# Kernel tuning notes

Measured on AMD Instinct MI355X. Metric: run time of the kernel, lower is better.

## Reference

```python
import jax, jax.numpy as jnp
import numpy as np

T, B, D = 512, 32, 1024

def setup_inputs() -> dict:
    key = jax.random.key(0)
    ks = jax.random.split(key, 4)
    scale = 1.0 / np.sqrt(D)
    x = jax.random.normal(ks[0], (T, B, D), dtype=jnp.float32)
    h0 = jnp.zeros((B, D), dtype=jnp.float32)
    W_alpha = jax.random.normal(ks[1], (D, D), dtype=jnp.float32) * scale
    b_alpha = jnp.zeros((D,), dtype=jnp.float32)
    # W_h in torch is orthogonal * 0.3; approximate with scaled gaussian of matching norm
    W_h = jax.random.normal(ks[2], (D, D), dtype=jnp.float32) * (0.3 * scale)
    W_x = jax.random.normal(ks[3], (D, D), dtype=jnp.float32) * scale
    b = jnp.zeros((D,), dtype=jnp.float32)
    return {"x": x, "h0": h0, "W_alpha": W_alpha, "b_alpha": b_alpha,
            "W_h": W_h, "W_x": W_x, "b": b}

def reference(x, h0, W_alpha, b_alpha, W_h, W_x, b):
    # Precompute input-dependent projections for all timesteps (batched GEMM)
    alpha_x_all = jnp.einsum('tbd,ed->tbe', x, W_alpha) + b_alpha  # [T,B,D]
    Wx_all = jnp.einsum('tbd,ed->tbe', x, W_x)                     # [T,B,D]

    def step(h_prev, inp):
        alpha_x_t, wx_t = inp
        alpha = jax.nn.sigmoid(alpha_x_t)
        v = jnp.tanh(h_prev @ W_h.T + wx_t + b)
        h_new = h_prev + alpha * v  # residual: identity path always present
        return h_new, h_new

    _, h_seq = jax.lax.scan(step, h0, (alpha_x_all, Wx_all))  # [T,B,D]
    h = jnp.concatenate([h0[None], h_seq], axis=0)            # [T+1,B,D]
    output = h_seq * jax.nn.silu(h_seq)                       # h * silu(h)
    return output, h
```

## Files before the change

kernel.cpp:

```cpp
#include <hip/hip_runtime.h>

typedef __bf16 bf16x8 __attribute__((ext_vector_type(8)));
typedef float  f32x4  __attribute__((ext_vector_type(4)));
typedef unsigned short u16;
typedef unsigned int   u32;
typedef unsigned long long u64;
typedef u16 u16x8 __attribute__((ext_vector_type(8)));

#define TT 512
#define BB 32
#define DD 1024

#define WS_Z   0
#define WS_HX  134217728
#define WS_FLG (134217728+262144)

static __device__ __forceinline__ u16 f2b(float f){
  u32 u = __builtin_bit_cast(u32, f);
  u32 r = (u + 0x7fffu + ((u>>16)&1u)) >> 16;
  return (u16)r;
}
static __device__ __forceinline__ float b2f(u16 h){
  return __builtin_bit_cast(float, (u32)h<<16);
}

#define AL32(p)   __hip_atomic_load((p),      __ATOMIC_RELAXED, __HIP_MEMORY_SCOPE_AGENT)
#define AL64(p)   __hip_atomic_load((p),      __ATOMIC_RELAXED, __HIP_MEMORY_SCOPE_AGENT)
#define AS32(p,v) __hip_atomic_store((p),(v), __ATOMIC_RELAXED, __HIP_MEMORY_SCOPE_AGENT)

#define MFMA16(a,b,c) __builtin_amdgcn_mfma_f32_16x16x32_bf16(a,b,c,0,0,0)

__global__ __launch_bounds__(256) void k_gemm3(const float* __restrict__ X,
    const float* __restrict__ Wa, const float* __restrict__ Wx,
    float* __restrict__ Z){
  __shared__ u16 Ahi[128*64];
  __shared__ u16 Alo[128*64];
  __shared__ u16 Bhi[128*64];
  __shared__ u16 Blo[128*64];
  int id  = blockIdx.x;
  int swz = (id & 7)*256 + (id>>3);
  int mblk = swz>>4, nblk = swz&15;
  const float* W = (nblk < 8) ? Wa : Wx;
  int n0 = (nblk&7)*128;
  int m0 = mblk*128;
  int tid = threadIdx.x, lane = tid&63, w = tid>>6;
  int wm = w>>1, wn = w&1;
  int sr = tid>>1, sh = tid&1;

  f32x4 acc[4][4];
  #pragma unroll
  for (int i=0;i<4;i++)
    #pragma unroll
    for (int j=0;j<4;j++) acc[i][j] = (f32x4){0.f,0.f,0.f,0.f};

  for (int kb = 0; kb < DD; kb += 64){
    const float* sa  = X + (size_t)(m0+sr)*DD + kb + sh*32;
    const float* sbp = W + (size_t)(n0+sr)*DD + kb + sh*32;
    int rswz = (sr&7)<<4;
    #pragma unroll
    for (int g=0; g<4; g++){
      float4 va0 = ((const float4*)sa)[g*2];
      float4 va1 = ((const float4*)sa)[g*2+1];
      float4 vb0 = ((const float4*)sbp)[g*2];
      float4 vb1 = ((const float4*)sbp)[g*2+1];
      float fa[8] = {va0.x,va0.y,va0.z,va0.w,va1.x,va1.y,va1.z,va1.w};
      float fb[8] = {vb0.x,vb0.y,vb0.z,vb0.w,vb1.x,vb1.y,vb1.z,vb1.w};
      u16x8 ah, al, bh, bl;
      #pragma unroll
      for (int j=0;j<8;j++){
        u16 ha = f2b(fa[j]); ah[j] = ha; al[j] = f2b(fa[j] - b2f(ha));
        u16 hb = f2b(fb[j]); bh[j] = hb; bl[j] = f2b(fb[j] - b2f(hb));
      }
      int off = sr*128 + ((sh*64 + g*16) ^ rswz);
      *(u16x8*)((char*)Ahi + off) = ah;
      *(u16x8*)((char*)Alo + off) = al;
      *(u16x8*)((char*)Bhi + off) = bh;
      *(u16x8*)((char*)Blo + off) = bl;
    }
    __syncthreads();
    #pragma unroll
    for (int ks=0; ks<2; ks++){
      int kby = ks*64 + ((lane>>4)<<4);
      bf16x8 ahf[4], alf[4], bhf[4], blf[4];
      #pragma unroll
      for (int mi=0;mi<4;mi++){
        int row = wm*64 + mi*16 + (lane&15);
        int ao = row*128 + (kby ^ ((row&7)<<4));
        ahf[mi] = *(const bf16x8*)((const char*)Ahi + ao);
        alf[mi] = *(const bf16x8*)((const char*)Alo + ao);
      }
      #pragma unroll
      for (int ni=0;ni<4;ni++){
        int row = wn*64 + ni*16 + (lane&15);
        int bo = row*128 + (kby ^ ((row&7)<<4));
        bhf[ni] = *(const bf16x8*)((const char*)Bhi + bo);
        blf[ni] = *(const bf16x8*)((const char*)Blo + bo);
      }
      #pragma unroll
      for (int mi=0;mi<4;mi++)
        #pragma unroll
        for (int ni=0;ni<4;ni++){
          acc[mi][ni] = MFMA16(ahf[mi], bhf[ni], acc[mi][ni]);
          acc[mi][ni] = MFMA16(ahf[mi], blf[ni], acc[mi][ni]);
          acc[mi][ni] = MFMA16(alf[mi], bhf[ni], acc[mi][ni]);
        }
    }
    __syncthreads();
  }

  #pragma unroll
  for (int mi=0;mi<4;mi++){
    #pragma unroll
    for (int ni=0;ni<4;ni++){
      int colz = nblk*128 + wn*64 + ni*16 + (lane&15);
      #pragma unroll
      for (int q=0;q<4;q++){
        int rowm = m0 + wm*64 + mi*16 + ((lane>>4)<<2) + q;
        Z[(size_t)rowm*2048 + colz] = acc[mi][ni][q];
      }
    }
  }
}

__global__ void k_init(const float* __restrict__ h0, float* __restrict__ hout0,
                       u32* __restrict__ hx, u32* __restrict__ flg){
  int i = blockIdx.x*blockDim.x + threadIdx.x;
  if (i < BB*DD){
    float v = h0[i];
    hout0[i] = v;
    u16 hh = f2b(v);
    u16 ll = f2b(v - b2f(hh));
    hx[i] = (u32)hh | ((u32)ll<<16);
  }
  if (i < 32) flg[i] = 0u;
  if (i == 32) flg[1024] = 0u;
}

#define UNPK(c, A, B) do { \
  u16x8 hi8, lo8; \
  hi8[0]=(u16)A.x; lo8[0]=(u16)(A.x>>16); \
  hi8[1]=(u16)A.y; lo8[1]=(u16)(A.y>>16); \
  hi8[2]=(u16)A.z; lo8[2]=(u16)(A.z>>16); \
  hi8[3]=(u16)A.w; lo8[3]=(u16)(A.w>>16); \
  hi8[4]=(u16)B.x; lo8[4]=(u16)(B.x>>16); \
  hi8[5]=(u16)B.y; lo8[5]=(u16)(B.y>>16); \
  hi8[6]=(u16)B.z; lo8[6]=(u16)(B.z>>16); \
  hi8[7]=(u16)B.w; lo8[7]=(u16)(B.w>>16); \
  int off_ = srow*2048 + ((kseg*128 + (c)*16) ^ ssw); \
  *(u16x8*)((char*)Hhi + off_) = hi8; \
  *(u16x8*)((char*)Hlo + off_) = lo8; \
} while(0)

__global__ __launch_bounds__(512, 2) void k_recur9(
    const float* __restrict__ Z, const float* __restrict__ Wh,
    const float* __restrict__ h0,
    const float* __restrict__ balpha, const float* __restrict__ bvec,
    float* __restrict__ out0,
    float* __restrict__ hout,
    u32* __restrict__ hx,
    u32* __restrict__ flg){
  __shared__ u16 Hhi[BB*DD];
  __shared__ u16 Hlo[BB*DD];
  __shared__ f32x4 Red[4][64];
  __shared__ int sdone;

  int blk = blockIdx.x;
  int tid = threadIdx.x, lane = tid&63, w = tid>>6;

  if (blk >= 32){
    if (tid == 0) sdone = 0;
    __syncthreads();
    float a = (float)tid + 1.0f;
    float m = 1.000001f, c = 0.9999991f;
    for (;;){
      for (int i = 0; i < 512; i++){
        asm volatile("v_fmac_f32 %0, %1, %2" : "+v"(a) : "v"(m), "v"(c));
      }
      if (tid == 0) sdone = (int)AL32(flg + 1024);
      __syncthreads();
      if (sdone) break;
      __syncthreads();
    }
    asm volatile("" :: "v"(a));
    return;
  }

  int e0 = blk*32;
  int kh = w>>2, wm = (w>>1)&1, wn = w&1;

  bf16x8 wfh[16], wfl[16];
  {
    const float* wrow = Wh + (size_t)(e0 + wn*16 + (lane&15))*DD
                           + kh*512 + ((lane>>4)<<3);
    #pragma unroll
    for (int ks=0; ks<16; ks++){
      float4 a = ((const float4*)(wrow + ks*32))[0];
      float4 b = ((const float4*)(wrow + ks*32))[1];
      float f[8] = {a.x,a.y,a.z,a.w,b.x,b.y,b.z,b.w};
      u16x8 uh, ul;
      #pragma unroll
      for (int j=0;j<8;j++){
        u16 hh = f2b(f[j]);
        uh[j] = hh;
        ul[j] = f2b(f[j] - b2f(hh));
      }
      wfh[ks] = __builtin_bit_cast(bf16x8, uh);
      wfl[ks] = __builtin_bit_cast(bf16x8, ul);
    }
  }

  int el = e0 + wn*16 + (lane&15);
  float ba = balpha[el], bb = bvec[el];
  float hc[4]  = {0.f,0.f,0.f,0.f};
  float ov[4]  = {0.f,0.f,0.f,0.f};
  float axr[4] = {0.f,0.f,0.f,0.f};
  float wxr[4] = {0.f,0.f,0.f,0.f};
  if (kh == 0){
    #pragma unroll
    for (int q=0;q<4;q++){
      int b = wm*16 + ((lane>>4)<<2) + q;
      hc[q]  = h0[b*DD + el];
      axr[q] = Z[(size_t)b*2048 + el];
      wxr[q] = Z[(size_t)b*2048 + DD + el];
    }
  }

  int srow = tid & 31;
  int kseg = tid >> 5;
  int ssw  = (srow & 15) << 4;

  for (int t=0;t<TT;t++){
    if (tid < 16){
      const u64* fp = (const u64*)(flg + tid*2);
      u64 fl = AL64(fp);
      while ((u32)fl < (u32)t || (u32)(fl>>32) < (u32)t) fl = AL64(fp);
    }
    __syncthreads();

    const u32* hsrc = hx + (size_t)(t&1)*BB*DD;
    const void* gp = (const void*)(hsrc + srow*DD + kseg*64);
    uint4 r0,r1,r2,r3,r4,r5,r6,r7,r8,r9,rA,rB,rC,rD,rE,rF;
    asm volatile(
      "global_load_dwordx4 %0, %16, off sc1\n\t"
      "global_load_dwordx4 %1, %16, off offset:16 sc1\n\t"
      "global_load_dwordx4 %2, %16, off offset:32 sc1\n\t"
      "global_load_dwordx4 %3, %16, off offset:48 sc1\n\t"
      "global_load_dwordx4 %4, %16, off offset:64 sc1\n\t"
      "global_load_dwordx4 %5, %16, off offset:80 sc1\n\t"
      "global_load_dwordx4 %6, %16, off offset:96 sc1\n\t"
      "global_load_dwordx4 %7, %16, off offset:112 sc1\n\t"
      "global_load_dwordx4 %8, %16, off offset:128 sc1\n\t"
      "global_load_dwordx4 %9, %16, off offset:144 sc1\n\t"
      "global_load_dwordx4 %10, %16, off offset:160 sc1\n\t"
      "global_load_dwordx4 %11, %16, off offset:176 sc1\n\t"
      "global_load_dwordx4 %12, %16, off offset:192 sc1\n\t"
      "global_load_dwordx4 %13, %16, off offset:208 sc1\n\t"
      "global_load_dwordx4 %14, %16, off offset:224 sc1\n\t"
      "global_load_dwordx4 %15, %16, off offset:240 sc1\n\t"
      "s_waitcnt vmcnt(0)"
      : "=&v"(r0), "=&v"(r1), "=&v"(r2), "=&v"(r3),
        "=&v"(r4), "=&v"(r5), "=&v"(r6), "=&v"(r7),
        "=&v"(r8), "=&v"(r9), "=&v"(rA), "=&v"(rB),
        "=&v"(rC), "=&v"(rD), "=&v"(rE), "=&v"(rF)
      : "v"(gp)
      : "memory");
    UNPK(0, r0, r1);  UNPK(1, r2, r3);
    UNPK(2, r4, r5);  UNPK(3, r6, r7);
    UNPK(4, r8, r9);  UNPK(5, rA, rB);
    UNPK(6, rC, rD);  UNPK(7, rE, rF);

    float axc[4], wxc[4];
    if (kh == 0){
      #pragma unroll
      for (int q=0;q<4;q++){ axc[q]=axr[q]; wxc[q]=wxr[q]; }
      if (t < TT-1){
        #pragma unroll
        for (int q=0;q<4;q++){
          int b = wm*16 + ((lane>>4)<<2) + q;
          size_t zi = ((size_t)(t+1)*BB + b)*2048 + el;
          axr[q] = Z[zi]; wxr[q] = Z[zi + DD];
        }
      }
    } else {
      #pragma unroll
      for (int q=0;q<4;q++){ axc[q]=0.f; wxc[q]=0.f; }
    }
    __syncthreads();

    f32x4 a0 = (f32x4){0.f,0.f,0.f,0.f};
    f32x4 a1 = (f32x4){0.f,0.f,0.f,0.f};
    f32x4 a2 = (f32x4){0.f,0.f,0.f,0.f};
    int ra    = wm*16 + (lane&15);
    int rbase = ra*2048;
    int rsw   = (ra&15)<<4;
    int kb0   = kh*1024 + ((lane>>4)<<4);
    #pragma unroll
    for (int ks=0; ks<16; ks++){
      int off = rbase + ((kb0 + ks*64) ^ rsw);
      bf16x8 ahi = *(const bf16x8*)((const char*)Hhi + off);
      bf16x8 alo = *(const bf16x8*)((const char*)Hlo + off);
      a0 = MFMA16(ahi, wfh[ks], a0);
      a1 = MFMA16(ahi, wfl[ks], a1);
      a2 = MFMA16(alo, wfh[ks], a2);
    }
    f32x4 acc = a0 + a1 + a2;
    if (kh == 1){ Red[wm*2+wn][lane] = acc; }
    __syncthreads();

    if (kh == 0){
      acc += Red[wm*2+wn][lane];
      u32* hnx = hx + (size_t)((t+1)&1)*BB*DD;
      #pragma unroll
      for (int q=0;q<4;q++){
        int b = wm*16 + ((lane>>4)<<2) + q;
        float ax = axc[q] + ba;
        float alpha = 1.f/(1.f + __expf(-ax));
        float s  = acc[q] + wxc[q] + bb;
        float as = fabsf(s);
        float e2 = __expf(-2.f*as);
        float vv = __builtin_copysignf((1.f - e2)/(1.f + e2), s);
        float h = hc[q] + alpha*vv;
        hc[q] = h;
        float sg = 1.f/(1.f + __expf(-h));
        ov[q] = h*h*sg;
        u16 hh = f2b(h);
        u16 ll = f2b(h - b2f(hh));
        AS32(hnx + b*DD + el, (u32)hh | ((u32)ll<<16));
      }
    }

    __syncthreads();
    if (tid == 0) AS32(flg + blk, (u32)(t+1));

    if (kh == 0){
      #pragma unroll
      for (int q=0;q<4;q++){
        int b = wm*16 + ((lane>>4)<<2) + q;
        size_t oi = (size_t)t*(BB*DD) + (size_t)b*DD + el;
        out0[oi] = ov[q];
        hout[oi + BB*DD] = hc[q];
      }
    }
  }

  if (tid == 0) AS32(flg + 1024, 1u);
}

extern "C" void kernel_launch(void* const* d_in, const int* in_sizes, int n_in,
                              void* d_out, int out_size, void* d_ws, size_t ws_size,
                              hipStream_t stream){
  (void)in_sizes; (void)n_in; (void)out_size; (void)ws_size;
  const float* x   = (const float*)d_in[0];
  const float* h0  = (const float*)d_in[1];
  const float* Wa  = (const float*)d_in[2];
  const float* bal = (const float*)d_in[3];
  const float* Whf = (const float*)d_in[4];
  const float* Wxf = (const float*)d_in[5];
  const float* bv  = (const float*)d_in[6];

  char* ws = (char*)d_ws;
  float* Zb  = (float*)(ws + WS_Z);
  u32*   hx  = (u32*)(ws + WS_HX);
  u32*   flg = (u32*)(ws + WS_FLG);

  float* out0 = (float*)d_out;
  float* hout = (float*)d_out + (size_t)TT*BB*DD;

  k_gemm3<<<2048, 256, 0, stream>>>(x, Wa, Wxf, Zb);
  k_init<<<(BB*DD+255)/256, 256, 0, stream>>>(h0, hout, hx, flg);

  void* args[] = {(void*)&Zb, (void*)&Whf, (void*)&h0, (void*)&bal, (void*)&bv,
                  (void*)&out0, (void*)&hout, (void*)&hx, (void*)&flg};
  hipLaunchCooperativeKernel((const void*)k_recur9, dim3(256), dim3(512),
                             args, 0, stream);
}
```

Measured before the change: 4.600 ms.

## Use single atomic counter barrier and overlap output stores with h loads

Replaces the per-block flag array, which 16 threads polled, with one global counter. Each wave that writes h increments it with an atomic add, and a single thread spins until the count reaches 128*t. The output and h stores for step t-1 are now issued after the next step's h loads, using a partial vmcnt wait so they overlap load latency, and the final step is stored after the loop. This also drops one __syncthreads per step, but adds contention on one atomic address and a dummy scratch buffer for t=0.

```diff
diff --git a/kernel.cpp b/kernel.cpp
--- a/kernel.cpp
+++ b/kernel.cpp
@@ -10,10 +10,12 @@
 #define TT 512
 #define BB 32
 #define DD 1024
+#define BBDD (BB*DD)
 
 #define WS_Z   0
 #define WS_HX  134217728
 #define WS_FLG (134217728+262144)
+#define WS_DMY (134217728+262144+8192)
 
 static __device__ __forceinline__ u16 f2b(float f){
   u32 u = __builtin_bit_cast(u32, f);
@@ -25,7 +27,6 @@
 }
 
 #define AL32(p)   __hip_atomic_load((p),      __ATOMIC_RELAXED, __HIP_MEMORY_SCOPE_AGENT)
-#define AL64(p)   __hip_atomic_load((p),      __ATOMIC_RELAXED, __HIP_MEMORY_SCOPE_AGENT)
 #define AS32(p,v) __hip_atomic_store((p),(v), __ATOMIC_RELAXED, __HIP_MEMORY_SCOPE_AGENT)
 
 #define MFMA16(a,b,c) __builtin_amdgcn_mfma_f32_16x16x32_bf16(a,b,c,0,0,0)
@@ -132,8 +133,8 @@
     u16 ll = f2b(v - b2f(hh));
     hx[i] = (u32)hh | ((u32)ll<<16);
   }
-  if (i < 32) flg[i] = 0u;
-  if (i == 32) flg[1024] = 0u;
+  if (i == 0) flg[0] = 0u;
+  if (i == 1) flg[1024] = 0u;
 }
 
 #define UNPK(c, A, B) do { \
@@ -151,14 +152,15 @@
   *(u16x8*)((char*)Hlo + off_) = lo8; \
 } while(0)
 
-__global__ __launch_bounds__(512, 2) void k_recur9(
+__global__ __launch_bounds__(512, 2) void k_recur11(
     const float* __restrict__ Z, const float* __restrict__ Wh,
     const float* __restrict__ h0,
     const float* __restrict__ balpha, const float* __restrict__ bvec,
     float* __restrict__ out0,
     float* __restrict__ hout,
     u32* __restrict__ hx,
-    u32* __restrict__ flg){
+    u32* __restrict__ flg,
+    float* __restrict__ dmy){
   __shared__ u16 Hhi[BB*DD];
   __shared__ u16 Hlo[BB*DD];
   __shared__ f32x4 Red[4][64];
@@ -230,10 +232,10 @@
   int ssw  = (srow & 15) << 4;
 
   for (int t=0;t<TT;t++){
-    if (tid < 16){
-      const u64* fp = (const u64*)(flg + tid*2);
-      u64 fl = AL64(fp);
-      while ((u32)fl < (u32)t || (u32)(fl>>32) < (u32)t) fl = AL64(fp);
+    if (tid == 256){
+      u32 tgt = 128u*(u32)t;
+      u32 c = AL32(flg);
+      while (c < tgt) c = AL32(flg);
     }
     __syncthreads();
 
@@ -256,14 +258,29 @@
       "global_load_dwordx4 %12, %16, off offset:192 sc1\n\t"
       "global_load_dwordx4 %13, %16, off offset:208 sc1\n\t"
       "global_load_dwordx4 %14, %16, off offset:224 sc1\n\t"
-      "global_load_dwordx4 %15, %16, off offset:240 sc1\n\t"
-      "s_waitcnt vmcnt(0)"
+      "global_load_dwordx4 %15, %16, off offset:240 sc1"
       : "=&v"(r0), "=&v"(r1), "=&v"(r2), "=&v"(r3),
         "=&v"(r4), "=&v"(r5), "=&v"(r6), "=&v"(r7),
         "=&v"(r8), "=&v"(r9), "=&v"(rA), "=&v"(rB),
         "=&v"(rC), "=&v"(rD), "=&v"(rE), "=&v"(rF)
       : "v"(gp)
       : "memory");
+
+    if (kh == 0){
+      float* o0 = (t == 0) ? dmy : (out0 + (size_t)(t-1)*BBDD);
+      float* h1 = (t == 0) ? (dmy + BBDD/2) : (hout + (size_t)t*BBDD);
+      #pragma unroll
+      for (int q=0;q<4;q++){
+        int b = wm*16 + ((lane>>4)<<2) + q;
+        o0[b*DD + el] = ov[q];
+        h1[b*DD + el] = hc[q];
+      }
+      asm volatile("s_waitcnt vmcnt(8)" ::: "memory");
+    } else {
+      asm volatile("s_waitcnt vmcnt(0)" ::: "memory");
+    }
+    __builtin_amdgcn_sched_barrier(0);
+
     UNPK(0, r0, r1);  UNPK(1, r2, r3);
     UNPK(2, r4, r5);  UNPK(3, r6, r7);
     UNPK(4, r8, r9);  UNPK(5, rA, rB);
@@ -273,13 +290,12 @@
     if (kh == 0){
       #pragma unroll
       for (int q=0;q<4;q++){ axc[q]=axr[q]; wxc[q]=wxr[q]; }
-      if (t < TT-1){
-        #pragma unroll
-        for (int q=0;q<4;q++){
-          int b = wm*16 + ((lane>>4)<<2) + q;
-          size_t zi = ((size_t)(t+1)*BB + b)*2048 + el;
-          axr[q] = Z[zi]; wxr[q] = Z[zi + DD];
-        }
+      int tn = (t < TT-1) ? (t+1) : t;
+      #pragma unroll
+      for (int q=0;q<4;q++){
+        int b = wm*16 + ((lane>>4)<<2) + q;
+        size_t zi = ((size_t)tn*BB + b)*2048 + el;
+        axr[q] = Z[zi]; wxr[q] = Z[zi + DD];
       }
     } else {
       #pragma unroll
@@ -327,22 +343,22 @@
         u16 ll = f2b(h - b2f(hh));
         AS32(hnx + b*DD + el, (u32)hh | ((u32)ll<<16));
       }
-    }
-
-    __syncthreads();
-    if (tid == 0) AS32(flg + blk, (u32)(t+1));
-
-    if (kh == 0){
-      #pragma unroll
-      for (int q=0;q<4;q++){
-        int b = wm*16 + ((lane>>4)<<2) + q;
-        size_t oi = (size_t)t*(BB*DD) + (size_t)b*DD + el;
-        out0[oi] = ov[q];
-        hout[oi + BB*DD] = hc[q];
-      }
-    }
-  }
-
+      asm volatile("s_waitcnt vmcnt(0)" ::: "memory");
+      if (lane == 0)
+        __hip_atomic_fetch_add(flg, 1u, __ATOMIC_RELAXED,
+                               __HIP_MEMORY_SCOPE_AGENT);
+    }
+  }
+
+  if (blk < 32 && (w>>2) == 0){
+    #pragma unroll
+    for (int q=0;q<4;q++){
+      int b = ((w>>1)&1)*16 + ((lane>>4)<<2) + q;
+      size_t oi = (size_t)(TT-1)*BBDD + (size_t)b*DD + el;
+      out0[oi] = ov[q];
+      hout[oi + BBDD] = hc[q];
+    }
+  }
   if (tid == 0) AS32(flg + 1024, 1u);
 }
 
@@ -362,6 +378,7 @@
   float* Zb  = (float*)(ws + WS_Z);
   u32*   hx  = (u32*)(ws + WS_HX);
   u32*   flg = (u32*)(ws + WS_FLG);
+  float* dmy = (float*)(ws + WS_DMY);
 
   float* out0 = (float*)d_out;
   float* hout = (float*)d_out + (size_t)TT*BB*DD;
@@ -370,7 +387,8 @@
   k_init<<<(BB*DD+255)/256, 256, 0, stream>>>(h0, hout, hx, flg);
 
   void* args[] = {(void*)&Zb, (void*)&Whf, (void*)&h0, (void*)&bal, (void*)&bv,
-                  (void*)&out0, (void*)&hout, (void*)&hx, (void*)&flg};
-  hipLaunchCooperativeKernel((const void*)k_recur9, dim3(256), dim3(512),
+                  (void*)&out0, (void*)&hout, (void*)&hx, (void*)&flg,
+                  (void*)&dmy};
+  hipLaunchCooperativeKernel((const void*)k_recur11, dim3(256), dim3(512),
                              args, 0, stream);
 }
```

After: 6.068 ms. 1.32x slower.

## Split recurrence block into independent batch-half groups with fine-grained flags

Applied to the files above, without the earlier changes.

Each 32-column block is split into two independent 4-wave groups, each handling 16 batch rows, with its own shared staging buffers. Block-wide __syncthreads are replaced by LDS counters and per-wave spin waits. Each group polls per-(group,block,wn) global flags with wave-wide __all and s_sleep, so the two batch halves can advance through time steps without waiting on each other. The reduction handoff between K-halves uses counter/ack pairs. This adds spin overhead and memory-ordering risk in exchange for less synchronisation latency on the critical path.

```diff
diff --git a/kernel.cpp b/kernel.cpp
--- a/kernel.cpp
+++ b/kernel.cpp
@@ -10,6 +10,7 @@
 #define TT 512
 #define BB 32
 #define DD 1024
+#define BBDD (BB*DD)
 
 #define WS_Z   0
 #define WS_HX  134217728
@@ -24,8 +25,8 @@
   return __builtin_bit_cast(float, (u32)h<<16);
 }
 
+#define AL64(p)   __hip_atomic_load((p),      __ATOMIC_RELAXED, __HIP_MEMORY_SCOPE_AGENT)
 #define AL32(p)   __hip_atomic_load((p),      __ATOMIC_RELAXED, __HIP_MEMORY_SCOPE_AGENT)
-#define AL64(p)   __hip_atomic_load((p),      __ATOMIC_RELAXED, __HIP_MEMORY_SCOPE_AGENT)
 #define AS32(p,v) __hip_atomic_store((p),(v), __ATOMIC_RELAXED, __HIP_MEMORY_SCOPE_AGENT)
 
 #define MFMA16(a,b,c) __builtin_amdgcn_mfma_f32_16x16x32_bf16(a,b,c,0,0,0)
@@ -58,11 +59,11 @@
     const float* sbp = W + (size_t)(n0+sr)*DD + kb + sh*32;
     int rswz = (sr&7)<<4;
     #pragma unroll
-    for (int g=0; g<4; g++){
-      float4 va0 = ((const float4*)sa)[g*2];
-      float4 va1 = ((const float4*)sa)[g*2+1];
-      float4 vb0 = ((const float4*)sbp)[g*2];
-      float4 vb1 = ((const float4*)sbp)[g*2+1];
+    for (int gg=0; gg<4; gg++){
+      float4 va0 = ((const float4*)sa)[gg*2];
+      float4 va1 = ((const float4*)sa)[gg*2+1];
+      float4 vb0 = ((const float4*)sbp)[gg*2];
+      float4 vb1 = ((const float4*)sbp)[gg*2+1];
       float fa[8] = {va0.x,va0.y,va0.z,va0.w,va1.x,va1.y,va1.z,va1.w};
       float fb[8] = {vb0.x,vb0.y,vb0.z,vb0.w,vb1.x,vb1.y,vb1.z,vb1.w};
       u16x8 ah, al, bh, bl;
@@ -71,7 +72,7 @@
         u16 ha = f2b(fa[j]); ah[j] = ha; al[j] = f2b(fa[j] - b2f(ha));
         u16 hb = f2b(fb[j]); bh[j] = hb; bl[j] = f2b(fb[j] - b2f(hb));
       }
-      int off = sr*128 + ((sh*64 + g*16) ^ rswz);
+      int off = sr*128 + ((sh*64 + gg*16) ^ rswz);
       *(u16x8*)((char*)Ahi + off) = ah;
       *(u16x8*)((char*)Alo + off) = al;
       *(u16x8*)((char*)Bhi + off) = bh;
@@ -132,8 +133,8 @@
     u16 ll = f2b(v - b2f(hh));
     hx[i] = (u32)hh | ((u32)ll<<16);
   }
-  if (i < 32) flg[i] = 0u;
-  if (i == 32) flg[1024] = 0u;
+  if (i < 128) flg[i] = 0u;
+  if (i == 128) flg[1024] = 0u;
 }
 
 #define UNPK(c, A, B) do { \
@@ -146,12 +147,12 @@
   hi8[5]=(u16)B.y; lo8[5]=(u16)(B.y>>16); \
   hi8[6]=(u16)B.z; lo8[6]=(u16)(B.z>>16); \
   hi8[7]=(u16)B.w; lo8[7]=(u16)(B.w>>16); \
-  int off_ = srow*2048 + ((kseg*128 + (c)*16) ^ ssw); \
-  *(u16x8*)((char*)Hhi + off_) = hi8; \
-  *(u16x8*)((char*)Hlo + off_) = lo8; \
+  int off_ = srow*2048 + ((kby0 + (c)*16) ^ ssw); \
+  *(u16x8*)(HhiB + off_) = hi8; \
+  *(u16x8*)(HloB + off_) = lo8; \
 } while(0)
 
-__global__ __launch_bounds__(512, 2) void k_recur9(
+__global__ __launch_bounds__(512, 2) void k_recur13(
     const float* __restrict__ Z, const float* __restrict__ Wh,
     const float* __restrict__ h0,
     const float* __restrict__ balpha, const float* __restrict__ bvec,
@@ -159,9 +160,12 @@
     float* __restrict__ hout,
     u32* __restrict__ hx,
     u32* __restrict__ flg){
-  __shared__ u16 Hhi[BB*DD];
-  __shared__ u16 Hlo[BB*DD];
-  __shared__ f32x4 Red[4][64];
+  __shared__ u16 Hhi[2][16*1024];
+  __shared__ u16 Hlo[2][16*1024];
+  __shared__ f32x4 Red[2][2][64];
+  __shared__ u32 StgCnt[2];
+  __shared__ u32 RedCnt[2][2];
+  __shared__ u32 RedAck[2][2];
   __shared__ int sdone;
 
   int blk = blockIdx.x;
@@ -185,8 +189,17 @@
     return;
   }
 
+  int g  = w>>2;
+  int kh = (w>>1)&1;
+  int wn = w&1;
   int e0 = blk*32;
-  int kh = w>>2, wm = (w>>1)&1, wn = w&1;
+
+  if (tid == 0){
+    StgCnt[0]=0; StgCnt[1]=0;
+    RedCnt[0][0]=0; RedCnt[0][1]=0; RedCnt[1][0]=0; RedCnt[1][1]=0;
+    RedAck[0][0]=0; RedAck[0][1]=0; RedAck[1][0]=0; RedAck[1][1]=0;
+  }
+  __syncthreads();
 
   bf16x8 wfh[16], wfl[16];
   {
@@ -212,33 +225,42 @@
   int el = e0 + wn*16 + (lane&15);
   float ba = balpha[el], bb = bvec[el];
   float hc[4]  = {0.f,0.f,0.f,0.f};
-  float ov[4]  = {0.f,0.f,0.f,0.f};
   float axr[4] = {0.f,0.f,0.f,0.f};
   float wxr[4] = {0.f,0.f,0.f,0.f};
   if (kh == 0){
     #pragma unroll
     for (int q=0;q<4;q++){
-      int b = wm*16 + ((lane>>4)<<2) + q;
+      int b = g*16 + ((lane>>4)<<2) + q;
       hc[q]  = h0[b*DD + el];
       axr[q] = Z[(size_t)b*2048 + el];
       wxr[q] = Z[(size_t)b*2048 + DD + el];
     }
   }
 
-  int srow = tid & 31;
-  int kseg = tid >> 5;
-  int ssw  = (srow & 15) << 4;
+  int srow  = lane&15;
+  int kbase = kh*512 + wn*256 + ((lane>>4)<<6);
+  int kby0  = kbase*2;
+  int ssw   = srow<<4;
+  char* HhiB = (char*)&Hhi[g][0];
+  char* HloB = (char*)&Hlo[g][0];
+  const u64* fp = (const u64*)(flg + g*64) + (lane&31);
+  volatile u32* stg = &StgCnt[g];
+  volatile u32* rcn = &RedCnt[g][wn];
+  volatile u32* rak = &RedAck[g][wn];
 
   for (int t=0;t<TT;t++){
-    if (tid < 16){
-      const u64* fp = (const u64*)(flg + tid*2);
-      u64 fl = AL64(fp);
-      while ((u32)fl < (u32)t || (u32)(fl>>32) < (u32)t) fl = AL64(fp);
-    }
-    __syncthreads();
-
-    const u32* hsrc = hx + (size_t)(t&1)*BB*DD;
-    const void* gp = (const void*)(hsrc + srow*DD + kseg*64);
+    {
+      u64 fv = AL64(fp);
+      int ok = ((u32)fv >= (u32)t) & ((u32)(fv>>32) >= (u32)t);
+      while (!__all(ok)){
+        __builtin_amdgcn_s_sleep(1);
+        fv = AL64(fp);
+        ok = ((u32)fv >= (u32)t) & ((u32)(fv>>32) >= (u32)t);
+      }
+    }
+
+    const u32* hsrc = hx + (size_t)(t&1)*BBDD;
+    const void* gp = (const void*)(hsrc + (g*16+srow)*DD + kbase);
     uint4 r0,r1,r2,r3,r4,r5,r6,r7,r8,r9,rA,rB,rC,rD,rE,rF;
     asm volatile(
       "global_load_dwordx4 %0, %16, off sc1\n\t"
@@ -264,58 +286,56 @@
         "=&v"(rC), "=&v"(rD), "=&v"(rE), "=&v"(rF)
       : "v"(gp)
       : "memory");
+    __builtin_amdgcn_sched_barrier(0);
     UNPK(0, r0, r1);  UNPK(1, r2, r3);
     UNPK(2, r4, r5);  UNPK(3, r6, r7);
     UNPK(4, r8, r9);  UNPK(5, rA, rB);
     UNPK(6, rC, rD);  UNPK(7, rE, rF);
 
-    float axc[4], wxc[4];
-    if (kh == 0){
-      #pragma unroll
-      for (int q=0;q<4;q++){ axc[q]=axr[q]; wxc[q]=wxr[q]; }
-      if (t < TT-1){
-        #pragma unroll
-        for (int q=0;q<4;q++){
-          int b = wm*16 + ((lane>>4)<<2) + q;
-          size_t zi = ((size_t)(t+1)*BB + b)*2048 + el;
-          axr[q] = Z[zi]; wxr[q] = Z[zi + DD];
-        }
-      }
-    } else {
-      #pragma unroll
-      for (int q=0;q<4;q++){ axc[q]=0.f; wxc[q]=0.f; }
-    }
-    __syncthreads();
+    asm volatile("s_waitcnt lgkmcnt(0)" ::: "memory");
+    if (lane == 0) atomicAdd((u32*)stg, 1u);
+    {
+      u32 tgt = 4u*(u32)(t+1);
+      while (*stg < tgt) __builtin_amdgcn_s_sleep(1);
+    }
+    __builtin_amdgcn_sched_barrier(0);
 
     f32x4 a0 = (f32x4){0.f,0.f,0.f,0.f};
     f32x4 a1 = (f32x4){0.f,0.f,0.f,0.f};
     f32x4 a2 = (f32x4){0.f,0.f,0.f,0.f};
-    int ra    = wm*16 + (lane&15);
-    int rbase = ra*2048;
-    int rsw   = (ra&15)<<4;
+    int rbase = (lane&15)*2048;
+    int rsw   = (lane&15)<<4;
     int kb0   = kh*1024 + ((lane>>4)<<4);
     #pragma unroll
     for (int ks=0; ks<16; ks++){
       int off = rbase + ((kb0 + ks*64) ^ rsw);
-      bf16x8 ahi = *(const bf16x8*)((const char*)Hhi + off);
-      bf16x8 alo = *(const bf16x8*)((const char*)Hlo + off);
+      bf16x8 ahi = *(const bf16x8*)(HhiB + off);
+      bf16x8 alo = *(const bf16x8*)(HloB + off);
       a0 = MFMA16(ahi, wfh[ks], a0);
       a1 = MFMA16(ahi, wfl[ks], a1);
       a2 = MFMA16(alo, wfh[ks], a2);
     }
     f32x4 acc = a0 + a1 + a2;
-    if (kh == 1){ Red[wm*2+wn][lane] = acc; }
-    __syncthreads();
-
-    if (kh == 0){
-      acc += Red[wm*2+wn][lane];
-      u32* hnx = hx + (size_t)((t+1)&1)*BB*DD;
+
+    if (kh == 1){
+      while (*rak < (u32)t) __builtin_amdgcn_s_sleep(1);
+      Red[g][wn][lane] = acc;
+      asm volatile("s_waitcnt lgkmcnt(0)" ::: "memory");
+      if (lane == 0) *rcn = (u32)(t+1);
+    } else {
+      while (*rcn < (u32)(t+1)) __builtin_amdgcn_s_sleep(1);
+      acc += Red[g][wn][lane];
+      asm volatile("s_waitcnt lgkmcnt(0)" ::: "memory");
+      if (lane == 0) *rak = (u32)(t+1);
+
+      float ov[4];
+      u32* hnx = hx + (size_t)((t+1)&1)*BBDD;
       #pragma unroll
       for (int q=0;q<4;q++){
-        int b = wm*16 + ((lane>>4)<<2) + q;
-        float ax = axc[q] + ba;
+        int b = g*16 + ((lane>>4)<<2) + q;
+        float ax = axr[q] + ba;
         float alpha = 1.f/(1.f + __expf(-ax));
-        float s  = acc[q] + wxc[q] + bb;
+        float s  = acc[q] + wxr[q] + bb;
         float as = fabsf(s);
         float e2 = __expf(-2.f*as);
         float vv = __builtin_copysignf((1.f - e2)/(1.f + e2), s);
@@ -327,23 +347,28 @@
         u16 ll = f2b(h - b2f(hh));
         AS32(hnx + b*DD + el, (u32)hh | ((u32)ll<<16));
       }
-    }
-
-    __syncthreads();
-    if (tid == 0) AS32(flg + blk, (u32)(t+1));
-
-    if (kh == 0){
+      asm volatile("s_waitcnt vmcnt(0)" ::: "memory");
+      if (lane == 0) AS32(flg + g*64 + blk*2 + wn, (u32)(t+1));
+
       #pragma unroll
       for (int q=0;q<4;q++){
-        int b = wm*16 + ((lane>>4)<<2) + q;
-        size_t oi = (size_t)t*(BB*DD) + (size_t)b*DD + el;
+        int b = g*16 + ((lane>>4)<<2) + q;
+        size_t oi = (size_t)t*BBDD + (size_t)b*DD + el;
         out0[oi] = ov[q];
-        hout[oi + BB*DD] = hc[q];
-      }
-    }
-  }
-
-  if (tid == 0) AS32(flg + 1024, 1u);
+        hout[oi + BBDD] = hc[q];
+      }
+      if (t < TT-1){
+        #pragma unroll
+        for (int q=0;q<4;q++){
+          int b = g*16 + ((lane>>4)<<2) + q;
+          size_t zi = ((size_t)(t+1)*BB + b)*2048 + el;
+          axr[q] = Z[zi]; wxr[q] = Z[zi + DD];
+        }
+      }
+    }
+  }
+
+  if (blk == 0 && tid == 0) AS32(flg + 1024, 1u);
 }
 
 extern "C" void kernel_launch(void* const* d_in, const int* in_sizes, int n_in,
@@ -371,6 +396,6 @@
 
   void* args[] = {(void*)&Zb, (void*)&Whf, (void*)&h0, (void*)&bal, (void*)&bv,
                   (void*)&out0, (void*)&hout, (void*)&hx, (void*)&flg};
-  hipLaunchCooperativeKernel((const void*)k_recur9, dim3(256), dim3(512),
+  hipLaunchCooperativeKernel((const void*)k_recur13, dim3(256), dim3(512),
                              args, 0, stream);
 }
```

New measurement: 7.106 ms. +54.5%, slower.

## Halve recurrence worker blocks to 16, each computing 64 columns over full batch

Applied to the files above, without the earlier changes.

The persistent recurrence now uses 16 worker blocks, each owning 64 output columns, instead of 32 blocks owning 32 columns. Each warp covers both batch halves with two MFMA fragment sets, and only 8 flag pairs are polled per step. The aim is to cut the cross-block synchronisation fan-in and the redundant per-block reloads of the full hidden state. The cost is twice the per-block MFMA and epilogue work on the serial critical path, plus more register pressure.

```diff
diff --git a/kernel.cpp b/kernel.cpp
--- a/kernel.cpp
+++ b/kernel.cpp
@@ -10,10 +10,12 @@
 #define TT 512
 #define BB 32
 #define DD 1024
+#define BBDD (BB*DD)
+#define NWB 16
 
 #define WS_Z   0
 #define WS_HX  134217728
-#define WS_FLG (134217728+262144)
+#define WS_FLG 134479872
 
 static __device__ __forceinline__ u16 f2b(float f){
   u32 u = __builtin_bit_cast(u32, f);
@@ -132,8 +134,8 @@
     u16 ll = f2b(v - b2f(hh));
     hx[i] = (u32)hh | ((u32)ll<<16);
   }
-  if (i < 32) flg[i] = 0u;
-  if (i == 32) flg[1024] = 0u;
+  if (i < NWB) flg[i] = 0u;
+  if (i == NWB) flg[1024] = 0u;
 }
 
 #define UNPK(c, A, B) do { \
@@ -151,7 +153,33 @@
   *(u16x8*)((char*)Hlo + off_) = lo8; \
 } while(0)
 
-__global__ __launch_bounds__(512, 2) void k_recur9(
+#define BURST16_SC1(GP) \
+    asm volatile( \
+      "global_load_dwordx4 %0, %16, off sc1\n\t" \
+      "global_load_dwordx4 %1, %16, off offset:16 sc1\n\t" \
+      "global_load_dwordx4 %2, %16, off offset:32 sc1\n\t" \
+      "global_load_dwordx4 %3, %16, off offset:48 sc1\n\t" \
+      "global_load_dwordx4 %4, %16, off offset:64 sc1\n\t" \
+      "global_load_dwordx4 %5, %16, off offset:80 sc1\n\t" \
+      "global_load_dwordx4 %6, %16, off offset:96 sc1\n\t" \
+      "global_load_dwordx4 %7, %16, off offset:112 sc1\n\t" \
+      "global_load_dwordx4 %8, %16, off offset:128 sc1\n\t" \
+      "global_load_dwordx4 %9, %16, off offset:144 sc1\n\t" \
+      "global_load_dwordx4 %10, %16, off offset:160 sc1\n\t" \
+      "global_load_dwordx4 %11, %16, off offset:176 sc1\n\t" \
+      "global_load_dwordx4 %12, %16, off offset:192 sc1\n\t" \
+      "global_load_dwordx4 %13, %16, off offset:208 sc1\n\t" \
+      "global_load_dwordx4 %14, %16, off offset:224 sc1\n\t" \
+      "global_load_dwordx4 %15, %16, off offset:240 sc1\n\t" \
+      "s_waitcnt vmcnt(0)" \
+      : "=&v"(r0), "=&v"(r1), "=&v"(r2), "=&v"(r3), \
+        "=&v"(r4), "=&v"(r5), "=&v"(r6), "=&v"(r7), \
+        "=&v"(r8), "=&v"(r9), "=&v"(rA), "=&v"(rB), \
+        "=&v"(rC), "=&v"(rD), "=&v"(rE), "=&v"(rF) \
+      : "v"(GP) \
+      : "memory")
+
+__global__ __launch_bounds__(512, 2) void k_recur15(
     const float* __restrict__ Z, const float* __restrict__ Wh,
     const float* __restrict__ h0,
     const float* __restrict__ balpha, const float* __restrict__ bvec,
@@ -161,13 +189,13 @@
     u32* __restrict__ flg){
   __shared__ u16 Hhi[BB*DD];
   __shared__ u16 Hlo[BB*DD];
-  __shared__ f32x4 Red[4][64];
+  __shared__ f32x4 Red[4][2][64];
   __shared__ int sdone;
 
   int blk = blockIdx.x;
   int tid = threadIdx.x, lane = tid&63, w = tid>>6;
 
-  if (blk >= 32){
+  if (blk >= NWB){
     if (tid == 0) sdone = 0;
     __syncthreads();
     float a = (float)tid + 1.0f;
@@ -185,8 +213,8 @@
     return;
   }
 
-  int e0 = blk*32;
-  int kh = w>>2, wm = (w>>1)&1, wn = w&1;
+  int e0 = blk*64;
+  int kh = w>>2, wn = w&3;
 
   bf16x8 wfh[16], wfl[16];
   {
@@ -211,18 +239,22 @@
 
   int el = e0 + wn*16 + (lane&15);
   float ba = balpha[el], bb = bvec[el];
-  float hc[4]  = {0.f,0.f,0.f,0.f};
-  float ov[4]  = {0.f,0.f,0.f,0.f};
-  float axr[4] = {0.f,0.f,0.f,0.f};
-  float wxr[4] = {0.f,0.f,0.f,0.f};
+  float hc[2][4], ov[2][4], axr[2][4], wxr[2][4];
+  #pragma unroll
+  for (int fr=0;fr<2;fr++)
+    #pragma unroll
+    for (int q=0;q<4;q++){ hc[fr][q]=0.f; ov[fr][q]=0.f;
+                           axr[fr][q]=0.f; wxr[fr][q]=0.f; }
   if (kh == 0){
     #pragma unroll
-    for (int q=0;q<4;q++){
-      int b = wm*16 + ((lane>>4)<<2) + q;
-      hc[q]  = h0[b*DD + el];
-      axr[q] = Z[(size_t)b*2048 + el];
-      wxr[q] = Z[(size_t)b*2048 + DD + el];
-    }
+    for (int fr=0;fr<2;fr++)
+      #pragma unroll
+      for (int q=0;q<4;q++){
+        int b = fr*16 + ((lane>>4)<<2) + q;
+        hc[fr][q]  = h0[b*DD + el];
+        axr[fr][q] = Z[(size_t)b*2048 + el];
+        wxr[fr][q] = Z[(size_t)b*2048 + DD + el];
+      }
   }
 
   int srow = tid & 31;
@@ -230,116 +262,111 @@
   int ssw  = (srow & 15) << 4;
 
   for (int t=0;t<TT;t++){
-    if (tid < 16){
+    if (tid < 8){
       const u64* fp = (const u64*)(flg + tid*2);
       u64 fl = AL64(fp);
       while ((u32)fl < (u32)t || (u32)(fl>>32) < (u32)t) fl = AL64(fp);
     }
     __syncthreads();
 
-    const u32* hsrc = hx + (size_t)(t&1)*BB*DD;
+    const u32* hsrc = hx + (size_t)(t&1)*BBDD;
     const void* gp = (const void*)(hsrc + srow*DD + kseg*64);
     uint4 r0,r1,r2,r3,r4,r5,r6,r7,r8,r9,rA,rB,rC,rD,rE,rF;
-    asm volatile(
-      "global_load_dwordx4 %0, %16, off sc1\n\t"
-      "global_load_dwordx4 %1, %16, off offset:16 sc1\n\t"
-      "global_load_dwordx4 %2, %16, off offset:32 sc1\n\t"
-      "global_load_dwordx4 %3, %16, off offset:48 sc1\n\t"
-      "global_load_dwordx4 %4, %16, off offset:64 sc1\n\t"
-      "global_load_dwordx4 %5, %16, off offset:80 sc1\n\t"
-      "global_load_dwordx4 %6, %16, off offset:96 sc1\n\t"
-      "global_load_dwordx4 %7, %16, off offset:112 sc1\n\t"
-      "global_load_dwordx4 %8, %16, off offset:128 sc1\n\t"
-      "global_load_dwordx4 %9, %16, off offset:144 sc1\n\t"
-      "global_load_dwordx4 %10, %16, off offset:160 sc1\n\t"
-      "global_load_dwordx4 %11, %16, off offset:176 sc1\n\t"
-      "global_load_dwordx4 %12, %16, off offset:192 sc1\n\t"
-      "global_load_dwordx4 %13, %16, off offset:208 sc1\n\t"
-      "global_load_dwordx4 %14, %16, off offset:224 sc1\n\t"
-      "global_load_dwordx4 %15, %16, off offset:240 sc1\n\t"
-      "s_waitcnt vmcnt(0)"
-      : "=&v"(r0), "=&v"(r1), "=&v"(r2), "=&v"(r3),
-        "=&v"(r4), "=&v"(r5), "=&v"(r6), "=&v"(r7),
-        "=&v"(r8), "=&v"(r9), "=&v"(rA), "=&v"(rB),
-        "=&v"(rC), "=&v"(rD), "=&v"(rE), "=&v"(rF)
-      : "v"(gp)
-      : "memory");
+    BURST16_SC1(gp);
     UNPK(0, r0, r1);  UNPK(1, r2, r3);
     UNPK(2, r4, r5);  UNPK(3, r6, r7);
     UNPK(4, r8, r9);  UNPK(5, rA, rB);
     UNPK(6, rC, rD);  UNPK(7, rE, rF);
 
-    float axc[4], wxc[4];
+    float axc[2][4], wxc[2][4];
     if (kh == 0){
       #pragma unroll
-      for (int q=0;q<4;q++){ axc[q]=axr[q]; wxc[q]=wxr[q]; }
+      for (int fr=0;fr<2;fr++)
+        #pragma unroll
+        for (int q=0;q<4;q++){ axc[fr][q]=axr[fr][q]; wxc[fr][q]=wxr[fr][q]; }
       if (t < TT-1){
         #pragma unroll
+        for (int fr=0;fr<2;fr++)
+          #pragma unroll
+          for (int q=0;q<4;q++){
+            int b = fr*16 + ((lane>>4)<<2) + q;
+            size_t zi = ((size_t)(t+1)*BB + b)*2048 + el;
+            axr[fr][q] = Z[zi]; wxr[fr][q] = Z[zi + DD];
+          }
+      }
+    } else {
+      #pragma unroll
+      for (int fr=0;fr<2;fr++)
+        #pragma unroll
+        for (int q=0;q<4;q++){ axc[fr][q]=0.f; wxc[fr][q]=0.f; }
+    }
+    __syncthreads();
+
+    f32x4 c00=(f32x4){0.f,0.f,0.f,0.f}, c01=c00, c02=c00;
+    f32x4 c10=c00, c11=c00, c12=c00;
+    int r0b = (lane&15)*2048;
+    int r1b = (16+(lane&15))*2048;
+    int rsw = (lane&15)<<4;
+    int kb0 = kh*1024 + ((lane>>4)<<4);
+    #pragma unroll
+    for (int ks=0; ks<16; ks++){
+      int co = (kb0 + ks*64) ^ rsw;
+      bf16x8 a0h = *(const bf16x8*)((const char*)Hhi + r0b + co);
+      bf16x8 a0l = *(const bf16x8*)((const char*)Hlo + r0b + co);
+      bf16x8 a1h = *(const bf16x8*)((const char*)Hhi + r1b + co);
+      bf16x8 a1l = *(const bf16x8*)((const char*)Hlo + r1b + co);
+      c00 = MFMA16(a0h, wfh[ks], c00);
+      c10 = MFMA16(a1h, wfh[ks], c10);
+      c01 = MFMA16(a0h, wfl[ks], c01);
+      c11 = MFMA16(a1h, wfl[ks], c11);
+      c02 = MFMA16(a0l, wfh[ks], c02);
+      c12 = MFMA16(a1l, wfh[ks], c12);
+    }
+    f32x4 aF0 = c00 + c01 + c02;
+    f32x4 aF1 = c10 + c11 + c12;
+    if (kh == 1){ Red[wn][0][lane] = aF0; Red[wn][1][lane] = aF1; }
+    __syncthreads();
+
+    if (kh == 0){
+      aF0 += Red[wn][0][lane];
+      aF1 += Red[wn][1][lane];
+      u32* hnx = hx + (size_t)((t+1)&1)*BBDD;
+      f32x4 af[2] = {aF0, aF1};
+      #pragma unroll
+      for (int fr=0;fr<2;fr++){
+        #pragma unroll
         for (int q=0;q<4;q++){
-          int b = wm*16 + ((lane>>4)<<2) + q;
-          size_t zi = ((size_t)(t+1)*BB + b)*2048 + el;
-          axr[q] = Z[zi]; wxr[q] = Z[zi + DD];
+          int b = fr*16 + ((lane>>4)<<2) + q;
+          float ax = axc[fr][q] + ba;
+          float alpha = 1.f/(1.f + __expf(-ax));
+          float s  = af[fr][q] + wxc[fr][q] + bb;
+          float as = fabsf(s);
+          float e2 = __expf(-2.f*as);
+          float vv = __builtin_copysignf((1.f - e2)/(1.f + e2), s);
+          float h = hc[fr][q] + alpha*vv;
+          hc[fr][q] = h;
+          float sg = 1.f/(1.f + __expf(-h));
+          ov[fr][q] = h*h*sg;
+          u16 hh = f2b(h);
+          u16 ll = f2b(h - b2f(hh));
+          AS32(hnx + b*DD + el, (u32)hh | ((u32)ll<<16));
         }
       }
-    } else {
-      #pragma unroll
-      for (int q=0;q<4;q++){ axc[q]=0.f; wxc[q]=0.f; }
-    }
-    __syncthreads();
-
-    f32x4 a0 = (f32x4){0.f,0.f,0.f,0.f};
-    f32x4 a1 = (f32x4){0.f,0.f,0.f,0.f};
-    f32x4 a2 = (f32x4){0.f,0.f,0.f,0.f};
-    int ra    = wm*16 + (lane&15);
-    int rbase = ra*2048;
-    int rsw   = (ra&15)<<4;
-    int kb0   = kh*1024 + ((lane>>4)<<4);
-    #pragma unroll
-    for (int ks=0; ks<16; ks++){
-      int off = rbase + ((kb0 + ks*64) ^ rsw);
-      bf16x8 ahi = *(const bf16x8*)((const char*)Hhi + off);
-      bf16x8 alo = *(const bf16x8*)((const char*)Hlo + off);
-      a0 = MFMA16(ahi, wfh[ks], a0);
-      a1 = MFMA16(ahi, wfl[ks], a1);
-      a2 = MFMA16(alo, wfh[ks], a2);
-    }
-    f32x4 acc = a0 + a1 + a2;
-    if (kh == 1){ Red[wm*2+wn][lane] = acc; }
-    __syncthreads();
+    }
+
+    __syncthreads();
+    if (tid == 0) AS32(flg + blk, (u32)(t+1));
 
     if (kh == 0){
-      acc += Red[wm*2+wn][lane];
-      u32* hnx = hx + (size_t)((t+1)&1)*BB*DD;
-      #pragma unroll
-      for (int q=0;q<4;q++){
-        int b = wm*16 + ((lane>>4)<<2) + q;
-        float ax = axc[q] + ba;
-        float alpha = 1.f/(1.f + __expf(-ax));
-        float s  = acc[q] + wxc[q] + bb;
-        float as = fabsf(s);
-        float e2 = __expf(-2.f*as);
-        float vv = __builtin_copysignf((1.f - e2)/(1.f + e2), s);
-        float h = hc[q] + alpha*vv;
-        hc[q] = h;
-        float sg = 1.f/(1.f + __expf(-h));
-        ov[q] = h*h*sg;
-        u16 hh = f2b(h);
-        u16 ll = f2b(h - b2f(hh));
-        AS32(hnx + b*DD + el, (u32)hh | ((u32)ll<<16));
-      }
-    }
-
-    __syncthreads();
-    if (tid == 0) AS32(flg + blk, (u32)(t+1));
-
-    if (kh == 0){
-      #pragma unroll
-      for (int q=0;q<4;q++){
-        int b = wm*16 + ((lane>>4)<<2) + q;
-        size_t oi = (size_t)t*(BB*DD) + (size_t)b*DD + el;
-        out0[oi] = ov[q];
-        hout[oi + BB*DD] = hc[q];
-      }
+      #pragma unroll
+      for (int fr=0;fr<2;fr++)
+        #pragma unroll
+        for (int q=0;q<4;q++){
+          int b = fr*16 + ((lane>>4)<<2) + q;
+          size_t oi = (size_t)t*BBDD + (size_t)b*DD + el;
+          out0[oi] = ov[fr][q];
+          hout[oi + BBDD] = hc[fr][q];
+        }
     }
   }
 
@@ -371,6 +398,6 @@
 
   void* args[] = {(void*)&Zb, (void*)&Whf, (void*)&h0, (void*)&bal, (void*)&bv,
                   (void*)&out0, (void*)&hout, (void*)&hx, (void*)&flg};
-  hipLaunchCooperativeKernel((const void*)k_recur9, dim3(256), dim3(512),
+  hipLaunchCooperativeKernel((const void*)k_recur15, dim3(256), dim3(512),
                              args, 0, stream);
 }
```

Measured after the change: 5.657 ms. 1.23x slower.
